# Optimization experiments

Measured on AMD Instinct MI355X. Metric: run time of the kernel, lower is better.

Reference implementation:

```python
import jax, jax.numpy as jnp
import numpy as np
from functools import partial

S, N, G2, R, E, IN, OUT = 32, 400, 16, 128, 64, 2, 5


def setup_inputs() -> dict:
    key = jax.random.key(0)
    ks = jax.random.split(key, 16)
    sc = lambda *sh: 1.0 / np.sqrt(sh[-1] if len(sh) > 1 else sh[0])
    return {
        "input_data": jax.random.normal(ks[0], (S, N, IN), jnp.float32),
        "grids": jax.random.uniform(ks[1], (S, N, N, G2), jnp.float32) * (jax.random.uniform(ks[2], (S, N, N, G2)) < 0.05),  # mostly-sparse grid masks
        "hidden_states": jax.random.normal(ks[3], (N, R), jnp.float32) * 0.1,
        "cell_states": jax.random.normal(ks[4], (N, R), jnp.float32) * 0.1,
        "W_in": jax.random.normal(ks[5], (IN, E), jnp.float32) * 0.5,
        "b_in": jax.random.normal(ks[6], (E,), jnp.float32) * 0.1,
        "W_t": jax.random.normal(ks[7], (G2 * R, E), jnp.float32) / np.sqrt(G2 * R),
        "b_t": jax.random.normal(ks[8], (E,), jnp.float32) * 0.1,
        "W_ih": jax.random.normal(ks[9], (4 * R, 2 * E), jnp.float32) / np.sqrt(2 * E),
        "b_ih": jax.random.normal(ks[10], (4 * R,), jnp.float32) * 0.1,
        "W_hh": jax.random.normal(ks[11], (4 * R, R), jnp.float32) / np.sqrt(R),
        "b_hh": jax.random.normal(ks[12], (4 * R,), jnp.float32) * 0.1,
        "W_out": jax.random.normal(ks[13], (R, OUT), jnp.float32) / np.sqrt(R),
        "b_out": jax.random.normal(ks[14], (OUT,), jnp.float32) * 0.1,
    }


def reference(input_data, grids, hidden_states, cell_states, W_in, b_in, W_t, b_t,
              W_ih, b_ih, W_hh, b_hh, W_out, b_out):
    n = hidden_states.shape[0]

    def step(carry, frame):
        h, c = carry
        x_f, grid_f = frame  # [N,2], [N,N,G2]
        # social tensor: for each node, grid[node].T @ hidden  -> [N, G2, R]
        social = jnp.einsum('nmg,mr->ngr', grid_f, h).reshape(n, -1)
        input_emb = jax.nn.relu(x_f @ W_in + b_in)          # dropout = identity (eval)
        tensor_emb = jax.nn.relu(social @ W_t + b_t)
        z = jnp.concatenate([input_emb, tensor_emb], axis=1)  # [N, 2E]
        gates = z @ W_ih.T + b_ih + h @ W_hh.T + b_hh         # [N, 4R]
        i, f, g, o = jnp.split(gates, 4, axis=1)              # torch LSTMCell gate order
        c_new = jax.nn.sigmoid(f) * c + jax.nn.sigmoid(i) * jnp.tanh(g)
        h_new = jax.nn.sigmoid(o) * jnp.tanh(c_new)
        out = h_new @ W_out + b_out
        return (h_new, c_new), out

    (h_fin, c_fin), outputs = jax.lax.scan(step, (hidden_states, cell_states), (input_data, grids))
    return outputs, h_fin, c_fin  # outputs: [S, N, output_size]
```

## Files before the change

kernel.cpp:

```cpp
#include <hip/hip_runtime.h>
#include <hip/hip_bf16.h>
#include <cstdint>

#define S_   32
#define N_   400
#define G2_  16
#define R_   128
#define E_   64
#define KDIM (N_*G2_)
#define COLS 1536
#define CAP  448
#define NB   200
#define NT   512
#define BAR_OFF 27131904

__device__ __forceinline__ float sigmoidf_(float x) { return 1.0f / (1.0f + __expf(-x)); }

__device__ __forceinline__ void ast_u32(uint32_t* p, uint32_t v) {
    __hip_atomic_store(p, v, __ATOMIC_RELAXED, __HIP_MEMORY_SCOPE_AGENT);
}
__device__ __forceinline__ uint32_t ald_u32(const uint32_t* p) {
    return __hip_atomic_load(p, __ATOMIC_RELAXED, __HIP_MEMORY_SCOPE_AGENT);
}
__device__ __forceinline__ float bfext(uint32_t u, int hi) {
    return __uint_as_float(hi ? (u & 0xffff0000u) : (u << 16));
}
__device__ __forceinline__ uint32_t bf16rne(float f) {
    uint32_t b = __float_as_uint(f);
    b += 0x7fffu + ((b >> 16) & 1u);
    return b >> 16;
}

__device__ void gsync(unsigned* slots, unsigned ep)
{
    __syncthreads();
    const int t = threadIdx.x;
    if (t == 0)
        __hip_atomic_store(&slots[blockIdx.x << 1], ep,
                           __ATOMIC_RELAXED, __HIP_MEMORY_SCOPE_AGENT);
    if (t < NB) {
        while (__hip_atomic_load(&slots[t << 1], __ATOMIC_RELAXED,
                                 __HIP_MEMORY_SCOPE_AGENT) < ep)
            __builtin_amdgcn_s_sleep(2);
    }
    __syncthreads();
}

__global__ __launch_bounds__(256) void k_compact(
    const float* __restrict__ grids, uint32_t* __restrict__ pairs,
    int* __restrict__ counts)
{
    int wave = (blockIdx.x << 2) | (threadIdx.x >> 6);
    int lane = threadIdx.x & 63;
    for (int rr = 0; rr < 2; ++rr) {
        int row = wave*2 + rr;
        const float* src = grids + (size_t)row * KDIM;
        uint32_t*    dst = pairs + (size_t)row * CAP;
        int cnt = 0;
        for (int chunk = 0; chunk < KDIM; chunk += 64) {
            int idx = chunk + lane;
            float v = src[idx];
            bool nz = (v != 0.0f);
            unsigned long long mask = __ballot(nz);
            if (mask) {
                if (nz) {
                    int off = __popcll(mask & ((1ull << lane) - 1ull));
                    int pos = cnt + off;
                    if (pos < CAP)
                        dst[pos] = ((uint32_t)idx << 16) | bf16rne(v);
                }
                cnt += __popcll(mask);
            }
        }
        if (lane == 0) counts[row] = (cnt < CAP) ? cnt : CAP;
    }
}

struct FusedArgs {
    const float* x;
    const float* W_in;  const float* b_in;  const float* b_t;
    const float* W_t;   const float* W_hh;  const float* W_ih;
    const float* b_ih;  const float* b_hh;
    const float* h0;    const float* c0;
    const float* W_out; const float* b_out;
    uint32_t* WCh;
    uint32_t* WihTh;
    uint16_t* HG0; uint16_t* HG1;
    const uint32_t* pairs; const int* counts;
    float* out;
    unsigned* slots;
};

__device__ __forceinline__ void hg_update(
    const uint32_t* __restrict__ WCh, uint16_t* HGn, int n0, int t,
    const float hb[2][128])
{
    if (t >= 256) return;
    float acc[3][2][2] = {};
    #pragma unroll 4
    for (int r = 0; r < 128; ++r) {
        float h0v = hb[0][r], h1v = hb[1][r];
        const uint32_t* wr = WCh + r*768;
        #pragma unroll
        for (int k = 0; k < 3; ++k) {
            uint32_t wp = wr[t + (k << 8)];
            float w0 = bfext(wp, 0), w1 = bfext(wp, 1);
            acc[k][0][0] += w0*h0v; acc[k][0][1] += w0*h1v;
            acc[k][1][0] += w1*h0v; acc[k][1][1] += w1*h1v;
        }
    }
    #pragma unroll
    for (int k = 0; k < 3; ++k) {
        int c = 2*(t + (k << 8));
        #pragma unroll
        for (int row = 0; row < 2; ++row) {
            uint32_t d = bf16rne(acc[k][0][row]) | (bf16rne(acc[k][1][row]) << 16);
            ast_u32((uint32_t*)(HGn + (size_t)(n0+row)*COLS + c), d);
        }
    }
}

__global__ __launch_bounds__(512) void k_fused(FusedArgs a)
{
    const int b = blockIdx.x, t = threadIdx.x;
    const int w = t >> 6, lane = t & 63;
    const int n0 = b << 1;
    unsigned ep = 0;

    __shared__ float tp_part[8][64];
    __shared__ float z[2][128];
    __shared__ float gl[2][512];
    __shared__ float hb[2][128];
    __shared__ float cl[2][128];

    for (int i = b*NT + t; i < 128*768 + 64*512; i += NB*NT) {
        if (i < 128*768) {
            int r = i / 768, cp = i - r*768;
            int c0 = cp * 2;
            float v0, v1;
            if (c0 < 1024) {
                int g = c0 >> 6, e = c0 & 63;
                v0 = a.W_t[(g*128 + r)*64 + e];
                v1 = a.W_t[(g*128 + r)*64 + e + 1];
            } else {
                int j = c0 - 1024;
                v0 = a.W_hh[j*128 + r];
                v1 = a.W_hh[(j+1)*128 + r];
            }
            ast_u32(&a.WCh[i], bf16rne(v0) | (bf16rne(v1) << 16));
        } else {
            int i2 = i - 128*768;
            int e2 = i2 >> 9, j = i2 & 511;
            float v0 = a.W_ih[j*128 + 2*e2];
            float v1 = a.W_ih[j*128 + 2*e2 + 1];
            ast_u32(&a.WihTh[i2], bf16rne(v0) | (bf16rne(v1) << 16));
        }
    }
    if (t < 256) {
        int qn = t >> 7, r = t & 127;
        hb[qn][r] = a.h0[(n0 + qn)*R_ + r];
        cl[qn][r] = a.c0[(n0 + qn)*R_ + r];
    }
    gsync(a.slots, ++ep);
    hg_update(a.WCh, a.HG0, n0, t, hb);
    gsync(a.slots, ++ep);

    float bias_j = a.b_ih[t] + a.b_hh[t];
    float bt_e = 0, win0 = 0, win1 = 0, bin_e = 0;
    if (t < 128) {
        int e = t & 63;
        bt_e = a.b_t[e]; win0 = a.W_in[e]; win1 = a.W_in[64 + e]; bin_e = a.b_in[e];
    }

    for (int s = 0; s < S_; ++s) {
        const uint16_t* HGc = (s & 1) ? a.HG1 : a.HG0;
        uint16_t*       HGn = (s & 1) ? a.HG0 : a.HG1;

        {
            int qn = w >> 2, qq = w & 3;
            int row = s*N_ + n0 + qn;
            int cnt = a.counts[row];
            const uint32_t* P = a.pairs + (size_t)row * CAP;
            float acc[16];
            #pragma unroll
            for (int u = 0; u < 16; ++u) acc[u] = 0.0f;
            int nb16 = cnt >> 4;
            int lbase = lane & ~1, lodd = lane & 1;
            for (int bi = qq; bi < nb16; bi += 4) {
                const uint4* q4 = reinterpret_cast<const uint4*>(P + (bi << 4));
                uint4 qa = q4[0], qb = q4[1], qc = q4[2], qd = q4[3];
                uint32_t qs[16] = {qa.x,qa.y,qa.z,qa.w, qb.x,qb.y,qb.z,qb.w,
                                   qc.x,qc.y,qc.z,qc.w, qd.x,qd.y,qd.z,qd.w};
                float hv[16];
                #pragma unroll
                for (int u = 0; u < 16; ++u) {
                    const uint32_t* ap = (const uint32_t*)
                        (HGc + (size_t)(qs[u] >> 20)*COLS + ((qs[u] >> 16) & 15u)*64 + lbase);
                    hv[u] = bfext(ald_u32(ap), lodd);
                }
                #pragma unroll
                for (int u = 0; u < 16; ++u)
                    acc[u] += __uint_as_float(qs[u] << 16) * hv[u];
            }
            if (qq == 3) {
                for (int p = nb16 << 4; p < cnt; ++p) {
                    uint32_t q = P[p];
                    const uint32_t* ap = (const uint32_t*)
                        (HGc + (size_t)(q >> 20)*COLS + ((q >> 16) & 15u)*64 + lbase);
                    acc[0] += __uint_as_float(q << 16) * bfext(ald_u32(ap), lodd);
                }
            }
            #pragma unroll
            for (int u = 8; u < 16; ++u) acc[u - 8] += acc[u];
            #pragma unroll
            for (int u = 4; u < 8; ++u) acc[u - 4] += acc[u];
            tp_part[w][lane] = (acc[0] + acc[1]) + (acc[2] + acc[3]);
        }
        __syncthreads();

        if (t < 128) {
            int qn = t >> 6, e = t & 63;
            int row = s*N_ + n0 + qn;
            float tp = (tp_part[4*qn][e] + tp_part[4*qn+1][e])
                     + (tp_part[4*qn+2][e] + tp_part[4*qn+3][e]);
            z[qn][64 + e] = fmaxf(tp + bt_e, 0.0f);
            float x0 = a.x[row*2 + 0], x1 = a.x[row*2 + 1];
            z[qn][e] = fmaxf(x0*win0 + x1*win1 + bin_e, 0.0f);
        }
        __syncthreads();

        {
            float g0 = 0, g1 = 0;
            #pragma unroll 8
            for (int e2 = 0; e2 < 64; ++e2) {
                uint32_t wp = a.WihTh[(e2 << 9) + t];
                float w0 = bfext(wp, 0), w1 = bfext(wp, 1);
                g0 += z[0][2*e2]*w0 + z[0][2*e2+1]*w1;
                g1 += z[1][2*e2]*w0 + z[1][2*e2+1]*w1;
            }
            int gb = 1024 + (t & ~1), godd = t & 1;
            uint32_t u0 = ald_u32((const uint32_t*)(HGc + (size_t)n0*COLS + gb));
            uint32_t u1 = ald_u32((const uint32_t*)(HGc + (size_t)(n0+1)*COLS + gb));
            gl[0][t] = g0 + bias_j + bfext(u0, godd);
            gl[1][t] = g1 + bias_j + bfext(u1, godd);
        }
        __syncthreads();

        if (t < 256) {
            int qn = t >> 7, r = t & 127;
            float gi = gl[qn][r], gf = gl[qn][128 + r];
            float gg = gl[qn][256 + r], go = gl[qn][384 + r];
            float cn = sigmoidf_(gf)*cl[qn][r] + sigmoidf_(gi)*tanhf(gg);
            float hn = sigmoidf_(go)*tanhf(cn);
            cl[qn][r] = cn;
            hb[qn][r] = hn;
            if (s == S_ - 1) {
                int n = n0 + qn;
                a.out[S_*N_*5 + n*R_ + r]          = hn;
                a.out[S_*N_*5 + N_*R_ + n*R_ + r]  = cn;
            }
        }
        __syncthreads();

        if (s < S_ - 1) hg_update(a.WCh, HGn, n0, t, hb);
        if (t >= 480 && t < 490) {
            int tp = t - 480;
            int qn = tp / 5, o = tp - (tp/5)*5;
            float av = a.b_out[o];
            for (int r = 0; r < 128; ++r) av += hb[qn][r] * a.W_out[r*5 + o];
            a.out[(s*N_ + n0 + qn)*5 + o] = av;
        }
        if (s < S_ - 1) gsync(a.slots, ++ep);
    }
}

__global__ __launch_bounds__(256) void k_prep(
    const float* __restrict__ W_t, const float* __restrict__ W_hh,
    const float* __restrict__ W_ih, const float* __restrict__ h0,
    const float* __restrict__ c0,
    float* __restrict__ WC, float* __restrict__ WihT,
    float* __restrict__ h, float* __restrict__ c)
{
    const int total = 128*COLS + 128*512 + 2*N_*R_;
    for (int idx = blockIdx.x*256 + threadIdx.x; idx < total; idx += gridDim.x*256) {
        int i = idx;
        if (i < 128*COLS) {
            int r = i / COLS, col = i - r*COLS;
            float v;
            if (col < 1024) { int g = col >> 6, e = col & 63; v = W_t[(g*128 + r)*64 + e]; }
            else            { int j = col - 1024;             v = W_hh[j*128 + r]; }
            WC[i] = v;
        } else if (i < 128*COLS + 128*512) {
            i -= 128*COLS;
            int e = i / 512, j = i - e*512;
            WihT[i] = W_ih[j*128 + e];
        } else {
            i -= 128*COLS + 128*512;
            if (i < N_*R_) h[i] = h0[i];
            else           c[i - N_*R_] = c0[i - N_*R_];
        }
    }
}

__global__ __launch_bounds__(256) void k_hg(
    const float* __restrict__ h, const float* __restrict__ WC,
    float* __restrict__ HG)
{
    __shared__ float hs[8][128];
    int rt = blockIdx.x / 6, ct = blockIdx.x - rt*6;
    int rowbase = rt * 8, colbase = ct * 256;
    #pragma unroll
    for (int k = 0; k < 4; ++k) {
        int i = k*256 + threadIdx.x;
        hs[i >> 7][i & 127] = h[(rowbase + (i >> 7))*R_ + (i & 127)];
    }
    __syncthreads();
    float acc[8] = {0,0,0,0,0,0,0,0};
    int col = colbase + threadIdx.x;
    const float* wcp = WC + col;
    #pragma unroll 4
    for (int r = 0; r < 128; ++r) {
        float wv = wcp[r * COLS];
        #pragma unroll
        for (int i = 0; i < 8; ++i) acc[i] += hs[i][r] * wv;
    }
    #pragma unroll
    for (int i = 0; i < 8; ++i) HG[(rowbase + i)*COLS + col] = acc[i];
}

__global__ __launch_bounds__(256) void k_step(
    int s,
    const float* __restrict__ x,
    const float* __restrict__ W_in, const float* __restrict__ b_in,
    const float* __restrict__ b_t,
    const float* __restrict__ WihT, const float* __restrict__ b_ih,
    const float* __restrict__ b_hh,
    const float* __restrict__ HG,
    const uint32_t* __restrict__ pairs, const int* __restrict__ counts,
    float* __restrict__ h, float* __restrict__ c,
    const float* __restrict__ W_out, const float* __restrict__ b_out,
    float* __restrict__ out, int last)
{
    __shared__ float z[4][128];
    __shared__ float gl[4][512];
    __shared__ float hb[4][128];

    int w = threadIdx.x >> 6, lane = threadIdx.x & 63;
    int n = (blockIdx.x << 2) | w;
    int row = s * N_ + n;

    int cnt = counts[row];
    const uint32_t* P = pairs + (size_t)row * CAP;
    float acc[8] = {0,0,0,0,0,0,0,0};
    int p = 0;
    for (; p + 8 <= cnt; p += 8) {
        uint4 qa = *reinterpret_cast<const uint4*>(P + p);
        uint4 qb = *reinterpret_cast<const uint4*>(P + p + 4);
        uint32_t qs[8] = {qa.x, qa.y, qa.z, qa.w, qb.x, qb.y, qb.z, qb.w};
        #pragma unroll
        for (int u = 0; u < 8; ++u) {
            uint32_t q = qs[u];
            acc[u] += __uint_as_float(q << 16) *
                      HG[(q >> 20)*COLS + ((q >> 16) & 15u)*64 + lane];
        }
    }
    for (; p < cnt; ++p) {
        uint32_t q = P[p];
        acc[0] += __uint_as_float(q << 16) *
                  HG[(q >> 20)*COLS + ((q >> 16) & 15u)*64 + lane];
    }
    float tp = ((acc[0]+acc[1]) + (acc[2]+acc[3])) + ((acc[4]+acc[5]) + (acc[6]+acc[7]));

    z[w][64 + lane] = fmaxf(tp + b_t[lane], 0.0f);
    float x0 = x[row*2 + 0], x1 = x[row*2 + 1];
    z[w][lane] = fmaxf(x0*W_in[lane] + x1*W_in[64 + lane] + b_in[lane], 0.0f);
    __syncthreads();

    int j0 = threadIdx.x, j1 = threadIdx.x + 256;
    float g0[4] = {0,0,0,0}, g1[4] = {0,0,0,0};
    for (int e = 0; e < 128; ++e) {
        float w0 = WihT[e*512 + j0], w1 = WihT[e*512 + j1];
        #pragma unroll
        for (int q = 0; q < 4; ++q) {
            float zv = z[q][e];
            g0[q] += zv * w0;
            g1[q] += zv * w1;
        }
    }
    float bi0 = b_ih[j0] + b_hh[j0], bi1 = b_ih[j1] + b_hh[j1];
    #pragma unroll
    for (int q = 0; q < 4; ++q) {
        int nq = (blockIdx.x << 2) | q;
        gl[q][j0] = g0[q] + bi0 + HG[nq*COLS + 1024 + j0];
        gl[q][j1] = g1[q] + bi1 + HG[nq*COLS + 1024 + j1];
    }
    __syncthreads();

    #pragma unroll
    for (int rep = 0; rep < 2; ++rep) {
        int t = rep*256 + threadIdx.x;
        int q = t >> 7, r = t & 127;
        int nq = (blockIdx.x << 2) | q;
        float gi = gl[q][r], gf = gl[q][128 + r], gg = gl[q][256 + r], go = gl[q][384 + r];
        float cold = c[nq*R_ + r];
        float cn = sigmoidf_(gf)*cold + sigmoidf_(gi)*tanhf(gg);
        float hn = sigmoidf_(go)*tanhf(cn);
        c[nq*R_ + r] = cn;
        h[nq*R_ + r] = hn;
        hb[q][r] = hn;
        if (last) {
            out[S_*N_*5 + nq*R_ + r]            = hn;
            out[S_*N_*5 + N_*R_ + nq*R_ + r]    = cn;
        }
    }
    __syncthreads();

    if (threadIdx.x < 20) {
        int q = threadIdx.x / 5, o = threadIdx.x - (threadIdx.x / 5)*5;
        int nq = (blockIdx.x << 2) | q;
        float a = b_out[o];
        for (int r = 0; r < 128; ++r) a += hb[q][r] * W_out[r*5 + o];
        out[(s*N_ + nq)*5 + o] = a;
    }
}

extern "C" void kernel_launch(void* const* d_in, const int* in_sizes, int n_in,
                              void* d_out, int out_size, void* d_ws, size_t ws_size,
                              hipStream_t stream)
{
    const float* input_data = (const float*)d_in[0];
    const float* grids      = (const float*)d_in[1];
    const float* h0         = (const float*)d_in[2];
    const float* c0         = (const float*)d_in[3];
    const float* W_in       = (const float*)d_in[4];
    const float* b_in       = (const float*)d_in[5];
    const float* W_t        = (const float*)d_in[6];
    const float* b_t        = (const float*)d_in[7];
    const float* W_ih       = (const float*)d_in[8];
    const float* b_ih       = (const float*)d_in[9];
    const float* W_hh       = (const float*)d_in[10];
    const float* b_hh       = (const float*)d_in[11];
    const float* W_out      = (const float*)d_in[12];
    const float* b_out      = (const float*)d_in[13];
    float* out = (float*)d_out;

    char* ws = (char*)d_ws;
    uint32_t* WCh    = (uint32_t*)(ws + 0);
    uint32_t* WihTh  = (uint32_t*)(ws + 393216);
    uint16_t* HG0    = (uint16_t*)(ws + 524288);
    uint16_t* HG1    = (uint16_t*)(ws + 1753088);
    float*    WCf    = (float*)(ws + 0);
    float*    WihTf  = (float*)(ws + 786432);
    float*    HGf    = (float*)(ws + 1048576);
    float*    h      = (float*)(ws + 3506176);
    float*    c      = (float*)(ws + 3710976);
    int*      counts = (int*)  (ws + 3915776);
    uint32_t* pairs  = (uint32_t*)(ws + 4194304);
    unsigned* slots  = (unsigned*)(ws + BAR_OFF);

    hipMemsetAsync(ws + BAR_OFF, 0, 2048, stream);
    k_compact<<<dim3(1600), dim3(256), 0, stream>>>(grids, pairs, counts);

    FusedArgs fa;
    fa.x = input_data; fa.W_in = W_in; fa.b_in = b_in; fa.b_t = b_t;
    fa.W_t = W_t; fa.W_hh = W_hh; fa.W_ih = W_ih;
    fa.b_ih = b_ih; fa.b_hh = b_hh;
    fa.h0 = h0; fa.c0 = c0; fa.W_out = W_out; fa.b_out = b_out;
    fa.WCh = WCh; fa.WihTh = WihTh; fa.HG0 = HG0; fa.HG1 = HG1;
    fa.pairs = pairs; fa.counts = counts; fa.out = out;
    fa.slots = slots;

    void* kargs[] = { (void*)&fa };
    hipError_t err = hipLaunchCooperativeKernel((void*)k_fused, dim3(NB), dim3(NT),
                                                kargs, 0, stream);
    if (err != hipSuccess) {
        k_prep<<<dim3(512), dim3(256), 0, stream>>>(W_t, W_hh, W_ih, h0, c0, WCf, WihTf, h, c);
        k_hg<<<dim3(300), dim3(256), 0, stream>>>(h, WCf, HGf);
        for (int s = 0; s < S_; ++s) {
            k_step<<<dim3(100), dim3(256), 0, stream>>>(
                s, input_data, W_in, b_in, b_t, WihTf, b_ih, b_hh, HGf, pairs, counts,
                h, c, W_out, b_out, out, (int)(s == S_ - 1));
            if (s < S_ - 1)
                k_hg<<<dim3(300), dim3(256), 0, stream>>>(h, WCf, HGf);
        }
    }
}
```

Baseline: 919.2 us.

## Compute W_hh recurrence locally instead of via global HG buffer

Drops the W_hh columns from the precomputed h@[W_t|W_hh] table, so hg_update writes only the 1024 tensor columns. The block now computes h@W_hh^T itself from shared-memory h with a packed bf16 W_hh copy. The HG buffers shrink, and gathers switch from per-load agent-scope atomic loads to plain loads, relying on an acquire fence added after the grid barrier. This removes a third of the hg_update work and global traffic. In exchange the gate stage gets a second 64-step dot-product loop per thread, and plain loads depend on the fence for correctness.

```diff
diff --git a/kernel.cpp b/kernel.cpp
--- a/kernel.cpp
+++ b/kernel.cpp
@@ -8,6 +8,7 @@
 #define R_   128
 #define E_   64
 #define KDIM (N_*G2_)
+#define HCOL 1024
 #define COLS 1536
 #define CAP  448
 #define NB   200
@@ -19,8 +20,9 @@
 __device__ __forceinline__ void ast_u32(uint32_t* p, uint32_t v) {
     __hip_atomic_store(p, v, __ATOMIC_RELAXED, __HIP_MEMORY_SCOPE_AGENT);
 }
-__device__ __forceinline__ uint32_t ald_u32(const uint32_t* p) {
-    return __hip_atomic_load(p, __ATOMIC_RELAXED, __HIP_MEMORY_SCOPE_AGENT);
+__device__ __forceinline__ void astf(float* p, float v) {
+    __hip_atomic_store((uint32_t*)p, __float_as_uint(v),
+                       __ATOMIC_RELAXED, __HIP_MEMORY_SCOPE_AGENT);
 }
 __device__ __forceinline__ float bfext(uint32_t u, int hi) {
     return __uint_as_float(hi ? (u & 0xffff0000u) : (u << 16));
@@ -44,6 +46,7 @@
             __builtin_amdgcn_s_sleep(2);
     }
     __syncthreads();
+    __builtin_amdgcn_fence(__ATOMIC_ACQUIRE, "agent");
 }
 
 __global__ __launch_bounds__(256) void k_compact(
@@ -85,24 +88,25 @@
     const float* W_out; const float* b_out;
     uint32_t* WCh;
     uint32_t* WihTh;
-    uint16_t* HG0; uint16_t* HG1;
+    uint32_t* WhhP;
+    uint32_t* HG0; uint32_t* HG1;
     const uint32_t* pairs; const int* counts;
     float* out;
     unsigned* slots;
 };
 
 __device__ __forceinline__ void hg_update(
-    const uint32_t* __restrict__ WCh, uint16_t* HGn, int n0, int t,
+    const uint32_t* __restrict__ WCh, uint32_t* HGn, int n0, int t,
     const float hb[2][128])
 {
     if (t >= 256) return;
-    float acc[3][2][2] = {};
+    float acc[2][2][2] = {};
     #pragma unroll 4
     for (int r = 0; r < 128; ++r) {
         float h0v = hb[0][r], h1v = hb[1][r];
-        const uint32_t* wr = WCh + r*768;
+        const uint32_t* wr = WCh + (r << 9);
         #pragma unroll
-        for (int k = 0; k < 3; ++k) {
+        for (int k = 0; k < 2; ++k) {
             uint32_t wp = wr[t + (k << 8)];
             float w0 = bfext(wp, 0), w1 = bfext(wp, 1);
             acc[k][0][0] += w0*h0v; acc[k][0][1] += w0*h1v;
@@ -110,12 +114,11 @@
         }
     }
     #pragma unroll
-    for (int k = 0; k < 3; ++k) {
-        int c = 2*(t + (k << 8));
+    for (int k = 0; k < 2; ++k) {
         #pragma unroll
         for (int row = 0; row < 2; ++row) {
             uint32_t d = bf16rne(acc[k][0][row]) | (bf16rne(acc[k][1][row]) << 16);
-            ast_u32((uint32_t*)(HGn + (size_t)(n0+row)*COLS + c), d);
+            ast_u32(HGn + ((size_t)(n0+row) << 9) + t + (k << 8), d);
         }
     }
 }
@@ -133,27 +136,25 @@
     __shared__ float hb[2][128];
     __shared__ float cl[2][128];
 
-    for (int i = b*NT + t; i < 128*768 + 64*512; i += NB*NT) {
-        if (i < 128*768) {
-            int r = i / 768, cp = i - r*768;
-            int c0 = cp * 2;
-            float v0, v1;
-            if (c0 < 1024) {
-                int g = c0 >> 6, e = c0 & 63;
-                v0 = a.W_t[(g*128 + r)*64 + e];
-                v1 = a.W_t[(g*128 + r)*64 + e + 1];
-            } else {
-                int j = c0 - 1024;
-                v0 = a.W_hh[j*128 + r];
-                v1 = a.W_hh[(j+1)*128 + r];
-            }
+    for (int i = b*NT + t; i < 65536 + 32768 + 32768; i += NB*NT) {
+        if (i < 65536) {
+            int r = i >> 9, cp = i & 511;
+            int c0 = cp * 2, g = c0 >> 6, e = c0 & 63;
+            float v0 = a.W_t[(g*128 + r)*64 + e];
+            float v1 = a.W_t[(g*128 + r)*64 + e + 1];
             ast_u32(&a.WCh[i], bf16rne(v0) | (bf16rne(v1) << 16));
-        } else {
-            int i2 = i - 128*768;
+        } else if (i < 98304) {
+            int i2 = i - 65536;
             int e2 = i2 >> 9, j = i2 & 511;
             float v0 = a.W_ih[j*128 + 2*e2];
             float v1 = a.W_ih[j*128 + 2*e2 + 1];
             ast_u32(&a.WihTh[i2], bf16rne(v0) | (bf16rne(v1) << 16));
+        } else {
+            int i3 = i - 98304;
+            int e2 = i3 >> 9, j = i3 & 511;
+            float v0 = a.W_hh[j*128 + 2*e2];
+            float v1 = a.W_hh[j*128 + 2*e2 + 1];
+            ast_u32(&a.WhhP[i3], bf16rne(v0) | (bf16rne(v1) << 16));
         }
     }
     if (t < 256) {
@@ -173,8 +174,8 @@
     }
 
     for (int s = 0; s < S_; ++s) {
-        const uint16_t* HGc = (s & 1) ? a.HG1 : a.HG0;
-        uint16_t*       HGn = (s & 1) ? a.HG0 : a.HG1;
+        const uint32_t* HGc = (s & 1) ? a.HG1 : a.HG0;
+        uint32_t*       HGn = (s & 1) ? a.HG0 : a.HG1;
 
         {
             int qn = w >> 2, qq = w & 3;
@@ -185,7 +186,7 @@
             #pragma unroll
             for (int u = 0; u < 16; ++u) acc[u] = 0.0f;
             int nb16 = cnt >> 4;
-            int lbase = lane & ~1, lodd = lane & 1;
+            int lhalf = lane >> 1, lodd = lane & 1;
             for (int bi = qq; bi < nb16; bi += 4) {
                 const uint4* q4 = reinterpret_cast<const uint4*>(P + (bi << 4));
                 uint4 qa = q4[0], qb = q4[1], qc = q4[2], qd = q4[3];
@@ -194,9 +195,9 @@
                 float hv[16];
                 #pragma unroll
                 for (int u = 0; u < 16; ++u) {
-                    const uint32_t* ap = (const uint32_t*)
-                        (HGc + (size_t)(qs[u] >> 20)*COLS + ((qs[u] >> 16) & 15u)*64 + lbase);
-                    hv[u] = bfext(ald_u32(ap), lodd);
+                    uint32_t q = qs[u];
+                    hv[u] = bfext(HGc[((size_t)(q >> 20) << 9) +
+                                      (((q >> 16) & 15u) << 5) + lhalf], lodd);
                 }
                 #pragma unroll
                 for (int u = 0; u < 16; ++u)
@@ -205,9 +206,9 @@
             if (qq == 3) {
                 for (int p = nb16 << 4; p < cnt; ++p) {
                     uint32_t q = P[p];
-                    const uint32_t* ap = (const uint32_t*)
-                        (HGc + (size_t)(q >> 20)*COLS + ((q >> 16) & 15u)*64 + lbase);
-                    acc[0] += __uint_as_float(q << 16) * bfext(ald_u32(ap), lodd);
+                    acc[0] += __uint_as_float(q << 16) *
+                              bfext(HGc[((size_t)(q >> 20) << 9) +
+                                        (((q >> 16) & 15u) << 5) + lhalf], lodd);
                 }
             }
             #pragma unroll
@@ -230,19 +231,20 @@
         __syncthreads();
 
         {
-            float g0 = 0, g1 = 0;
+            float g0 = 0, g1 = 0, gh0 = 0, gh1 = 0;
             #pragma unroll 8
             for (int e2 = 0; e2 < 64; ++e2) {
                 uint32_t wp = a.WihTh[(e2 << 9) + t];
+                uint32_t hp = a.WhhP [(e2 << 9) + t];
                 float w0 = bfext(wp, 0), w1 = bfext(wp, 1);
-                g0 += z[0][2*e2]*w0 + z[0][2*e2+1]*w1;
-                g1 += z[1][2*e2]*w0 + z[1][2*e2+1]*w1;
+                float u0 = bfext(hp, 0), u1 = bfext(hp, 1);
+                g0  += z[0][2*e2]*w0 + z[0][2*e2+1]*w1;
+                g1  += z[1][2*e2]*w0 + z[1][2*e2+1]*w1;
+                gh0 += hb[0][2*e2]*u0 + hb[0][2*e2+1]*u1;
+                gh1 += hb[1][2*e2]*u0 + hb[1][2*e2+1]*u1;
             }
-            int gb = 1024 + (t & ~1), godd = t & 1;
-            uint32_t u0 = ald_u32((const uint32_t*)(HGc + (size_t)n0*COLS + gb));
-            uint32_t u1 = ald_u32((const uint32_t*)(HGc + (size_t)(n0+1)*COLS + gb));
-            gl[0][t] = g0 + bias_j + bfext(u0, godd);
-            gl[1][t] = g1 + bias_j + bfext(u1, godd);
+            gl[0][t] = g0 + gh0 + bias_j;
+            gl[1][t] = g1 + gh1 + bias_j;
         }
         __syncthreads();
 
@@ -256,8 +258,8 @@
             hb[qn][r] = hn;
             if (s == S_ - 1) {
                 int n = n0 + qn;
-                a.out[S_*N_*5 + n*R_ + r]          = hn;
-                a.out[S_*N_*5 + N_*R_ + n*R_ + r]  = cn;
+                astf(&a.out[S_*N_*5 + n*R_ + r], hn);
+                astf(&a.out[S_*N_*5 + N_*R_ + n*R_ + r], cn);
             }
         }
         __syncthreads();
@@ -268,7 +270,7 @@
             int qn = tp / 5, o = tp - (tp/5)*5;
             float av = a.b_out[o];
             for (int r = 0; r < 128; ++r) av += hb[qn][r] * a.W_out[r*5 + o];
-            a.out[(s*N_ + n0 + qn)*5 + o] = av;
+            astf(&a.out[(s*N_ + n0 + qn)*5 + o], av);
         }
         if (s < S_ - 1) gsync(a.slots, ++ep);
     }
@@ -446,9 +448,10 @@
 
     char* ws = (char*)d_ws;
     uint32_t* WCh    = (uint32_t*)(ws + 0);
-    uint32_t* WihTh  = (uint32_t*)(ws + 393216);
-    uint16_t* HG0    = (uint16_t*)(ws + 524288);
-    uint16_t* HG1    = (uint16_t*)(ws + 1753088);
+    uint32_t* WihTh  = (uint32_t*)(ws + 262144);
+    uint32_t* WhhP   = (uint32_t*)(ws + 393216);
+    uint32_t* HG0    = (uint32_t*)(ws + 524288);
+    uint32_t* HG1    = (uint32_t*)(ws + 1343488);
     float*    WCf    = (float*)(ws + 0);
     float*    WihTf  = (float*)(ws + 786432);
     float*    HGf    = (float*)(ws + 1048576);
@@ -466,7 +469,8 @@
     fa.W_t = W_t; fa.W_hh = W_hh; fa.W_ih = W_ih;
     fa.b_ih = b_ih; fa.b_hh = b_hh;
     fa.h0 = h0; fa.c0 = c0; fa.W_out = W_out; fa.b_out = b_out;
-    fa.WCh = WCh; fa.WihTh = WihTh; fa.HG0 = HG0; fa.HG1 = HG1;
+    fa.WCh = WCh; fa.WihTh = WihTh; fa.WhhP = WhhP;
+    fa.HG0 = HG0; fa.HG1 = HG1;
     fa.pairs = pairs; fa.counts = counts; fa.out = out;
     fa.slots = slots;
 
```

Measured after the change: 1.454 ms. +58.2%, slower.
